# Optimization experiments

Measured on AMD Instinct MI355X. Metric: run time of the kernel, lower is better.

The kernel has to match this reference:

```python
import jax, jax.numpy as jnp
import numpy as np

N = 50000          # nodes
E = 1600000        # edges (avg degree 32)
D_MODEL = 128      # input == output dim
HEADS = 4
D_HEAD = D_MODEL // HEADS
N_LAYERS = 3


def _edge_softmax(scores, dst, n):
    # scores: [E, H]; softmax over edges sharing the same destination node
    m = jax.ops.segment_max(scores, dst, num_segments=n)          # [N, H]
    m = jnp.where(jnp.isfinite(m), m, 0.0)                        # empty segments -> -inf guard
    ex = jnp.exp(scores - m[dst])                                 # [E, H]
    denom = jax.ops.segment_sum(ex, dst, num_segments=n)          # [N, H]
    return ex / (denom[dst] + 1e-9)


def _gt_layer(h, src, dst, Wq, Wk, Wv, Wo):
    # h: [N, D]; one multi-head graph-attention (graph transformer) layer
    n = h.shape[0]
    q = (h @ Wq).reshape(n, HEADS, D_HEAD)
    k = (h @ Wk).reshape(n, HEADS, D_HEAD)
    v = (h @ Wv).reshape(n, HEADS, D_HEAD)
    scale = 1.0 / np.sqrt(D_HEAD).astype(np.float32)
    scores = jnp.einsum('ehd,ehd->eh', q[dst], k[src]) * scale    # [E, H]
    alpha = _edge_softmax(scores, dst, n)                         # [E, H]
    agg = jax.ops.segment_sum(alpha[:, :, None] * v[src], dst, num_segments=n)  # [N, H, Dh]
    return agg.reshape(n, D_MODEL) @ Wo


def setup_inputs() -> dict:
    key = jax.random.key(0)
    ks = jax.random.split(key, 16)
    s = 1.0 / np.sqrt(D_MODEL)
    inp = {
        'X':    jax.random.normal(ks[0], (N, 1), jnp.float32),
        'Seed': jax.random.uniform(ks[1], (N, 1), jnp.float32),
        'D':    jax.random.uniform(ks[2], (N, 1), jnp.float32),
        'C':    jax.random.uniform(ks[3], (N, 1), jnp.float32),
        'edge_src': jax.random.randint(ks[4], (E,), 0, N, jnp.int32),
        'edge_dst': jax.random.randint(ks[5], (E,), 0, N, jnp.int32),
        # scalar -> d_model embeddings (Linear(1, d, bias=False))
        'W_seed': jax.random.normal(ks[6], (1, D_MODEL), jnp.float32),
        'W_deg':  jax.random.normal(ks[7], (1, D_MODEL), jnp.float32),
        'W_clu':  jax.random.normal(ks[8], (1, D_MODEL), jnp.float32),
        # 3 graph-transformer layers
        'Wq': jax.random.normal(ks[9],  (N_LAYERS, D_MODEL, D_MODEL), jnp.float32) * s,
        'Wk': jax.random.normal(ks[10], (N_LAYERS, D_MODEL, D_MODEL), jnp.float32) * s,
        'Wv': jax.random.normal(ks[11], (N_LAYERS, D_MODEL, D_MODEL), jnp.float32) * s,
        'Wo': jax.random.normal(ks[12], (N_LAYERS, D_MODEL, D_MODEL), jnp.float32) * s,
        # MLP head: Linear(d,d)+ReLU, Linear(d,1)
        'W1': jax.random.normal(ks[13], (D_MODEL, D_MODEL), jnp.float32) * s,
        'b1': jnp.zeros((D_MODEL,), jnp.float32),
        'W2': jax.random.normal(ks[14], (D_MODEL, 1), jnp.float32) * s,
        'b2': jnp.zeros((1,), jnp.float32),
    }
    return inp


def reference(X, Seed, D, C, edge_src, edge_dst,
              W_seed, W_deg, W_clu, Wq, Wk, Wv, Wo, W1, b1, W2, b2):
    # faithful to original: raw X [N,1] broadcast-added to the embeddings
    h = X + Seed @ W_seed + D @ W_deg + C @ W_clu                 # [N, D_MODEL]
    for i in range(N_LAYERS):
        h = _gt_layer(h, edge_src, edge_dst, Wq[i], Wk[i], Wv[i], Wo[i])
    z = jax.nn.relu(h @ W1 + b1)
    return z @ W2 + b2                                            # [N, 1]
```

## Files before the change

### kernel.cpp

```cpp
#include <hip/hip_runtime.h>
#include <math.h>

#define DM 128
#define HEADS 4
#define DH 32
#define WSTRIDE 16384

typedef _Float16 f16x8 __attribute__((ext_vector_type(8)));
typedef _Float16 f16x4 __attribute__((ext_vector_type(4)));
typedef _Float16 f16x2 __attribute__((ext_vector_type(2)));
typedef float f32x4v __attribute__((ext_vector_type(4)));

__global__ void embed_kernel(const float* __restrict__ X, const float* __restrict__ Seed,
                             const float* __restrict__ Dg, const float* __restrict__ Cl,
                             const float* __restrict__ Wseed, const float* __restrict__ Wdeg,
                             const float* __restrict__ Wclu, float* __restrict__ H, int n) {
    int i = blockIdx.x * blockDim.x + threadIdx.x;
    if (i >= n * (DM / 4)) return;
    int nd = i >> 5, d4 = (i & 31) * 4;
    float x = X[nd], sd = Seed[nd], dg = Dg[nd], cl = Cl[nd];
    float4 ws = *reinterpret_cast<const float4*>(Wseed + d4);
    float4 wd = *reinterpret_cast<const float4*>(Wdeg + d4);
    float4 wc = *reinterpret_cast<const float4*>(Wclu + d4);
    float4 o;
    o.x = x + sd * ws.x + dg * wd.x + cl * wc.x;
    o.y = x + sd * ws.y + dg * wd.y + cl * wc.y;
    o.z = x + sd * ws.z + dg * wd.z + cl * wc.z;
    o.w = x + sd * ws.w + dg * wd.w + cl * wc.w;
    *reinterpret_cast<float4*>(H + nd * DM + d4) = o;
}

__global__ void count_kernel(const int* __restrict__ edst, int* __restrict__ deg, int E) {
    int e = blockIdx.x * blockDim.x + threadIdx.x;
    if (e < E) atomicAdd(&deg[edst[e]], 1);
}

__global__ void scan1_kernel(const int* __restrict__ in, int* __restrict__ outv,
                             int* __restrict__ bsums, int n) {
    __shared__ int s[256];
    int t = threadIdx.x;
    int i = blockIdx.x * 256 + t;
    int v = (i < n) ? in[i] : 0;
    s[t] = v;
    __syncthreads();
    for (int off = 1; off < 256; off <<= 1) {
        int x = (t >= off) ? s[t - off] : 0;
        __syncthreads();
        s[t] += x;
        __syncthreads();
    }
    if (i < n) outv[i] = s[t];
    if (t == 255) bsums[blockIdx.x] = s[255];
}

__global__ void scan2_kernel(int* __restrict__ bsums, int nb) {
    __shared__ int s[256];
    int t = threadIdx.x;
    int v = (t < nb) ? bsums[t] : 0;
    s[t] = v;
    __syncthreads();
    for (int off = 1; off < 256; off <<= 1) {
        int x = (t >= off) ? s[t - off] : 0;
        __syncthreads();
        s[t] += x;
        __syncthreads();
    }
    if (t < nb) bsums[t] = s[t];
}

__global__ void scan3_kernel(const int* __restrict__ outv, const int* __restrict__ bsums,
                             int* __restrict__ ptr, int n) {
    int i = blockIdx.x * 256 + threadIdx.x;
    if (i == 0) ptr[0] = 0;
    if (i < n) {
        int add = (blockIdx.x > 0) ? bsums[blockIdx.x - 1] : 0;
        ptr[i + 1] = outv[i] + add;
    }
}

__global__ void scatter_kernel(const int* __restrict__ esrc, const int* __restrict__ edst,
                               const int* __restrict__ ptr, int* __restrict__ fill,
                               int* __restrict__ out, int E) {
    int e = blockIdx.x * blockDim.x + threadIdx.x;
    if (e >= E) return;
    int d = edst[e];
    int pos = ptr[d] + atomicAdd(&fill[d], 1);
    out[pos] = esrc[e];
}

__global__ void prepack_kernel(const float* __restrict__ Wq, const float* __restrict__ Wk,
                               const float* __restrict__ Wv, const float* __restrict__ Wo,
                               const float* __restrict__ W1, _Float16* __restrict__ W16) {
    int m = blockIdx.z;
    const float* W;
    if (m < 3)       W = Wq + (size_t)m * DM * DM;
    else if (m < 6)  W = Wk + (size_t)(m - 3) * DM * DM;
    else if (m < 9)  W = Wv + (size_t)(m - 6) * DM * DM;
    else if (m < 12) W = Wo + (size_t)(m - 9) * DM * DM;
    else             W = W1;
    int kb = blockIdx.x, nb = blockIdx.y, l = threadIdx.x;
    int kbase = kb * 32 + (l >> 4) * 8;
    int c = nb * 16 + (l & 15);
    f16x8 v;
#pragma unroll
    for (int j = 0; j < 8; j++) v[j] = (_Float16)W[(kbase + j) * DM + c];
    *reinterpret_cast<f16x8*>(W16 + (size_t)m * WSTRIDE + ((kb * 8 + nb) * 64 + l) * 8) = v;
}

template <int OUT>
__global__ __launch_bounds__(256) void gemm_mfma_kernel(const float* __restrict__ A,
                                                        const _Float16* __restrict__ W16,
                                                        void* __restrict__ O, int ldO,
                                                        int colOff, int n) {
    __shared__ _Float16 sA[64 * 136];
    int t = threadIdx.x;
    int row0 = blockIdx.x * 64;
#pragma unroll
    for (int p = 0; p < 8; p++) {
        int f = p * 256 + t;
        int r = f >> 5, c4 = (f & 31) * 4;
        int gr = min(row0 + r, n - 1);
        float4 v = *reinterpret_cast<const float4*>(A + (size_t)gr * DM + c4);
        f16x4 h = {(_Float16)v.x, (_Float16)v.y, (_Float16)v.z, (_Float16)v.w};
        *reinterpret_cast<f16x4*>(&sA[r * 136 + c4]) = h;
    }
    __syncthreads();

    int w = t >> 6, l = t & 63;
    int lr = l & 15, lg = l >> 4;
    int rowb = w * 16;

    f32x4v acc[8];
#pragma unroll
    for (int nb = 0; nb < 8; nb++) acc[nb] = (f32x4v){0.f, 0.f, 0.f, 0.f};

#pragma unroll
    for (int kb = 0; kb < 4; kb++) {
        f16x8 a = *reinterpret_cast<const f16x8*>(&sA[(rowb + lr) * 136 + kb * 32 + lg * 8]);
#pragma unroll
        for (int nb = 0; nb < 8; nb++) {
            f16x8 b = *reinterpret_cast<const f16x8*>(&W16[((kb * 8 + nb) * 64 + l) * 8]);
            acc[nb] = __builtin_amdgcn_mfma_f32_16x16x32_f16(a, b, acc[nb], 0, 0, 0);
        }
    }

#pragma unroll
    for (int nb = 0; nb < 8; nb++) {
#pragma unroll
        for (int i = 0; i < 4; i++) {
            int r = row0 + rowb + lg * 4 + i;
            if (r >= n) continue;
            int c = nb * 16 + lr;
            if (OUT == 0) {
                ((float*)O)[(size_t)r * ldO + c] = acc[nb][i];
            } else {
                _Float16 h = (_Float16)acc[nb][i];
                ((unsigned short*)O)[(size_t)r * ldO + colOff + c] =
                    __builtin_bit_cast(unsigned short, h);
            }
        }
    }
}

__global__ __launch_bounds__(256) void attn_kernel(const float* __restrict__ Q,
                                                   const uint32_t* __restrict__ KV,
                                                   const int* __restrict__ ptr,
                                                   const int* __restrict__ esrc,
                                                   float* __restrict__ AGG, int n) {
    int w = threadIdx.x >> 6;
    int lane = threadIdx.x & 63;
    int node = blockIdx.x * 4 + w;
    if (node >= n) return;
    int e0 = ptr[node], e1 = ptr[node + 1];
    float2* outp = reinterpret_cast<float2*>(AGG + (size_t)node * DM + 2 * lane);
    if (e0 >= e1) {
        *outp = make_float2(0.f, 0.f);
        return;
    }
    const float scale = 0.17677669529663687f * 1.4426950408889634f;
    float2 qf = *reinterpret_cast<const float2*>(Q + (size_t)node * DM + 2 * lane);
    f16x2 qh = {(_Float16)qf.x, (_Float16)qf.y};

    float mA = -INFINITY, sA = 0.f, axA = 0.f, ayA = 0.f;
    float mB = -INFINITY, sB = 0.f, axB = 0.f, ayB = 0.f;

    int cnt = e1 - e0;
    int npairs = cnt >> 1;
    int last = e1 - 1;

    auto kvrow = [&](int src) { return KV + (size_t)src * 128; };

    int iA2 = 0, iB2 = 0;
    uint32_t kA0 = 0, vA0 = 0, kB0 = 0, vB0 = 0;
    uint32_t kA1 = 0, vA1 = 0, kB1 = 0, vB1 = 0;
    {
        int b0 = e0;
        int iA0 = esrc[min(b0, last)];
        int iB0 = esrc[min(b0 + 1, last)];
        const uint32_t* rA = kvrow(iA0);
        const uint32_t* rB = kvrow(iB0);
        kA0 = rA[lane]; vA0 = rA[64 + lane];
        kB0 = rB[lane]; vB0 = rB[64 + lane];
        int b1 = e0 + 2;
        int iA1 = esrc[min(b1, last)];
        int iB1 = esrc[min(b1 + 1, last)];
        const uint32_t* rA1 = kvrow(iA1);
        const uint32_t* rB1 = kvrow(iB1);
        kA1 = rA1[lane]; vA1 = rA1[64 + lane];
        kB1 = rB1[lane]; vB1 = rB1[64 + lane];
        int b2 = e0 + 4;
        iA2 = esrc[min(b2, last)];
        iB2 = esrc[min(b2 + 1, last)];
    }

#define PROC(kc, vc, m_, s_, ax_, ay_)                                         \
    {                                                                          \
        float p = __builtin_amdgcn_fdot2(qh, __builtin_bit_cast(f16x2, kc),    \
                                         0.f, false);                          \
        p += __shfl_xor(p, 1, 64);                                             \
        p += __shfl_xor(p, 2, 64);                                             \
        p += __shfl_xor(p, 4, 64);                                             \
        p += __shfl_xor(p, 8, 64);                                             \
        p *= scale;                                                            \
        float mn = fmaxf(m_, p);                                               \
        float dd = exp2f(m_ - mn);                                             \
        float wg = exp2f(p - mn);                                              \
        f16x2 vh = __builtin_bit_cast(f16x2, vc);                              \
        s_ = s_ * dd + wg;                                                     \
        ax_ = ax_ * dd + wg * (float)vh[0];                                    \
        ay_ = ay_ * dd + wg * (float)vh[1];                                    \
        m_ = mn;                                                               \
    }

    for (int p = 0; p < npairs; p++) {
        uint32_t kAc = kA0, vAc = vA0, kBc = kB0, vBc = vB0;
        kA0 = kA1; vA0 = vA1; kB0 = kB1; vB0 = vB1;
        const uint32_t* rA = kvrow(iA2);
        const uint32_t* rB = kvrow(iB2);
        kA1 = rA[lane]; vA1 = rA[64 + lane];
        kB1 = rB[lane]; vB1 = rB[64 + lane];
        int b = e0 + 2 * (p + 3);
        iA2 = esrc[min(b, last)];
        iB2 = esrc[min(b + 1, last)];
        PROC(kAc, vAc, mA, sA, axA, ayA);
        PROC(kBc, vBc, mB, sB, axB, ayB);
    }
    if (cnt & 1) {
        const uint32_t* r = kvrow(esrc[last]);
        uint32_t kc = r[lane], vc = r[64 + lane];
        PROC(kc, vc, mA, sA, axA, ayA);
    }
#undef PROC

    float mF = fmaxf(mA, mB);
    float dA = (mA > -INFINITY) ? exp2f(mA - mF) : 0.f;
    float dB = (mB > -INFINITY) ? exp2f(mB - mF) : 0.f;
    float s = sA * dA + sB * dB;
    float ax = axA * dA + axB * dB;
    float ay = ayA * dA + ayB * dB;
    float inv = 1.f / (s + 1e-9f);
    *outp = make_float2(ax * inv, ay * inv);
}

__global__ __launch_bounds__(256) void mlp_kernel(const float* __restrict__ H,
                                                  const _Float16* __restrict__ W16,
                                                  const float* __restrict__ b1,
                                                  const float* __restrict__ W2,
                                                  const float* __restrict__ b2,
                                                  float* __restrict__ out, int n) {
    __shared__ _Float16 sA[64 * 136];
    int t = threadIdx.x;
    int row0 = blockIdx.x * 64;
#pragma unroll
    for (int p = 0; p < 8; p++) {
        int f = p * 256 + t;
        int r = f >> 5, c4 = (f & 31) * 4;
        int gr = min(row0 + r, n - 1);
        float4 v = *reinterpret_cast<const float4*>(H + (size_t)gr * DM + c4);
        f16x4 h = {(_Float16)v.x, (_Float16)v.y, (_Float16)v.z, (_Float16)v.w};
        *reinterpret_cast<f16x4*>(&sA[r * 136 + c4]) = h;
    }
    __syncthreads();

    int w = t >> 6, l = t & 63;
    int lr = l & 15, lg = l >> 4;
    int rowb = w * 16;

    f32x4v acc[8];
#pragma unroll
    for (int nb = 0; nb < 8; nb++) acc[nb] = (f32x4v){0.f, 0.f, 0.f, 0.f};

#pragma unroll
    for (int kb = 0; kb < 4; kb++) {
        f16x8 a = *reinterpret_cast<const f16x8*>(&sA[(rowb + lr) * 136 + kb * 32 + lg * 8]);
#pragma unroll
        for (int nb = 0; nb < 8; nb++) {
            f16x8 b = *reinterpret_cast<const f16x8*>(&W16[((kb * 8 + nb) * 64 + l) * 8]);
            acc[nb] = __builtin_amdgcn_mfma_f32_16x16x32_f16(a, b, acc[nb], 0, 0, 0);
        }
    }

    float part[4] = {0.f, 0.f, 0.f, 0.f};
#pragma unroll
    for (int nb = 0; nb < 8; nb++) {
        int c = nb * 16 + lr;
        float b1v = b1[c];
        float w2v = W2[c];
#pragma unroll
        for (int i = 0; i < 4; i++) {
            float z = fmaxf(acc[nb][i] + b1v, 0.f);
            part[i] += z * w2v;
        }
    }
    float b2v = b2[0];
#pragma unroll
    for (int i = 0; i < 4; i++) {
        part[i] += __shfl_xor(part[i], 1, 64);
        part[i] += __shfl_xor(part[i], 2, 64);
        part[i] += __shfl_xor(part[i], 4, 64);
        part[i] += __shfl_xor(part[i], 8, 64);
        int r = row0 + rowb + lg * 4 + i;
        if (lr == 0 && r < n) out[r] = part[i] + b2v;
    }
}

extern "C" void kernel_launch(void* const* d_in, const int* in_sizes, int n_in,
                              void* d_out, int out_size, void* d_ws, size_t ws_size,
                              hipStream_t stream) {
    const float* X    = (const float*)d_in[0];
    const float* Seed = (const float*)d_in[1];
    const float* Dg   = (const float*)d_in[2];
    const float* Cl   = (const float*)d_in[3];
    const int* esrc   = (const int*)d_in[4];
    const int* edst   = (const int*)d_in[5];
    const float* Wseed = (const float*)d_in[6];
    const float* Wdeg  = (const float*)d_in[7];
    const float* Wclu  = (const float*)d_in[8];
    const float* Wq = (const float*)d_in[9];
    const float* Wk = (const float*)d_in[10];
    const float* Wv = (const float*)d_in[11];
    const float* Wo = (const float*)d_in[12];
    const float* W1 = (const float*)d_in[13];
    const float* b1 = (const float*)d_in[14];
    const float* W2 = (const float*)d_in[15];
    const float* b2 = (const float*)d_in[16];
    float* out = (float*)d_out;

    int n = in_sizes[0];
    int E = in_sizes[4];

    char* p = (char*)d_ws;
    auto alloc = [&](size_t bytes) {
        void* r = (void*)p;
        p += (bytes + 255) & ~(size_t)255;
        return r;
    };
    float* hbuf  = (float*)alloc((size_t)n * DM * 4);
    float* qbuf  = (float*)alloc((size_t)n * DM * 4);
    float* abuf  = (float*)alloc((size_t)n * DM * 4);
    unsigned short* kvbuf = (unsigned short*)alloc((size_t)n * 256 * 2);
    _Float16* W16 = (_Float16*)alloc((size_t)13 * WSTRIDE * 2);
    int* deg    = (int*)alloc((size_t)n * 4);
    int* ptr    = (int*)alloc((size_t)(n + 1) * 4);
    int* ptrtmp = (int*)alloc((size_t)n * 4);
    int* bsums  = (int*)alloc(1024);
    int* fill   = (int*)alloc((size_t)n * 4);
    int* esrcs  = (int*)alloc((size_t)E * 4);
    (void)ws_size; (void)n_in; (void)out_size;

    hipMemsetAsync(deg, 0, (size_t)n * 4, stream);
    hipMemsetAsync(fill, 0, (size_t)n * 4, stream);

    {
        int total = n * (DM / 4);
        embed_kernel<<<(total + 255) / 256, 256, 0, stream>>>(X, Seed, Dg, Cl, Wseed, Wdeg,
                                                              Wclu, hbuf, n);
    }
    int nb = (n + 255) / 256;
    count_kernel<<<(E + 255) / 256, 256, 0, stream>>>(edst, deg, E);
    scan1_kernel<<<nb, 256, 0, stream>>>(deg, ptrtmp, bsums, n);
    scan2_kernel<<<1, 256, 0, stream>>>(bsums, nb);
    scan3_kernel<<<nb, 256, 0, stream>>>(ptrtmp, bsums, ptr, n);
    scatter_kernel<<<(E + 255) / 256, 256, 0, stream>>>(esrc, edst, ptr, fill, esrcs, E);

    prepack_kernel<<<dim3(4, 8, 13), 64, 0, stream>>>(Wq, Wk, Wv, Wo, W1, W16);

    int ggrid = (n + 63) / 64;
    int agrid = (n + 3) / 4;
    for (int i = 0; i < 3; i++) {
        const _Float16* wq16 = W16 + (size_t)(0 + i) * WSTRIDE;
        const _Float16* wk16 = W16 + (size_t)(3 + i) * WSTRIDE;
        const _Float16* wv16 = W16 + (size_t)(6 + i) * WSTRIDE;
        const _Float16* wo16 = W16 + (size_t)(9 + i) * WSTRIDE;
        gemm_mfma_kernel<0><<<ggrid, 256, 0, stream>>>(hbuf, wq16, qbuf, DM, 0, n);
        gemm_mfma_kernel<1><<<ggrid, 256, 0, stream>>>(hbuf, wk16, kvbuf, 256, 0, n);
        gemm_mfma_kernel<1><<<ggrid, 256, 0, stream>>>(hbuf, wv16, kvbuf, 256, 128, n);
        attn_kernel<<<agrid, 256, 0, stream>>>(qbuf, (const uint32_t*)kvbuf, ptr, esrcs,
                                               abuf, n);
        gemm_mfma_kernel<0><<<ggrid, 256, 0, stream>>>(abuf, wo16, hbuf, DM, 0, n);
    }
    mlp_kernel<<<ggrid, 256, 0, stream>>>(hbuf, W16 + (size_t)12 * WSTRIDE, b1, W2, b2, out, n);
}
```

Measured before the change: 815.0 us.

## Process four edges per wavefront with 16-byte KV loads and lazy max rescaling

Restructures the attention kernel so each wavefront handles four edges at once, one per 16-lane quarter, with each lane holding 8 head dims loaded as uint4. The head dot-product reduction uses DPP xor adds over 4 lanes instead of four cross-lane shuffles, and the online-softmax running max is rescaled only when some new score exceeds it by more than a threshold. Partial softmax states are merged across quarters at the end. The aim is fewer shuffles, fewer exp calls and wider memory transactions per edge, at the cost of more registers and lane-divergent tail handling.

```diff
diff --git a/kernel.cpp b/kernel.cpp
--- a/kernel.cpp
+++ b/kernel.cpp
@@ -10,6 +10,15 @@
 typedef _Float16 f16x4 __attribute__((ext_vector_type(4)));
 typedef _Float16 f16x2 __attribute__((ext_vector_type(2)));
 typedef float f32x4v __attribute__((ext_vector_type(4)));
+
+__device__ __forceinline__ float dpp_xor1_add(float x) {
+    int r = __builtin_amdgcn_update_dpp(0, __builtin_bit_cast(int, x), 0xB1, 0xf, 0xf, true);
+    return x + __builtin_bit_cast(float, r);
+}
+__device__ __forceinline__ float dpp_xor2_add(float x) {
+    int r = __builtin_amdgcn_update_dpp(0, __builtin_bit_cast(int, x), 0x4E, 0xf, 0xf, true);
+    return x + __builtin_bit_cast(float, r);
+}
 
 __global__ void embed_kernel(const float* __restrict__ X, const float* __restrict__ Seed,
                              const float* __restrict__ Dg, const float* __restrict__ Cl,
@@ -167,99 +176,130 @@
                                                    const int* __restrict__ ptr,
                                                    const int* __restrict__ esrc,
                                                    float* __restrict__ AGG, int n) {
-    int w = threadIdx.x >> 6;
+    int wv = threadIdx.x >> 6;
     int lane = threadIdx.x & 63;
-    int node = blockIdx.x * 4 + w;
+    int node = blockIdx.x * 4 + wv;
     if (node >= n) return;
     int e0 = ptr[node], e1 = ptr[node + 1];
-    float2* outp = reinterpret_cast<float2*>(AGG + (size_t)node * DM + 2 * lane);
+    int q4 = lane >> 4;
+    int w = lane & 15;
+    float* outbase = AGG + (size_t)node * DM + 8 * w;
     if (e0 >= e1) {
-        *outp = make_float2(0.f, 0.f);
+        if (lane < 16) {
+            *reinterpret_cast<float4*>(outbase) = make_float4(0.f, 0.f, 0.f, 0.f);
+            *reinterpret_cast<float4*>(outbase + 4) = make_float4(0.f, 0.f, 0.f, 0.f);
+        }
         return;
     }
     const float scale = 0.17677669529663687f * 1.4426950408889634f;
-    float2 qf = *reinterpret_cast<const float2*>(Q + (size_t)node * DM + 2 * lane);
-    f16x2 qh = {(_Float16)qf.x, (_Float16)qf.y};
-
-    float mA = -INFINITY, sA = 0.f, axA = 0.f, ayA = 0.f;
-    float mB = -INFINITY, sB = 0.f, axB = 0.f, ayB = 0.f;
-
-    int cnt = e1 - e0;
-    int npairs = cnt >> 1;
+    float4 qa = *reinterpret_cast<const float4*>(Q + (size_t)node * DM + 8 * w);
+    float4 qb = *reinterpret_cast<const float4*>(Q + (size_t)node * DM + 8 * w + 4);
+    f16x2 qh0 = {(_Float16)(qa.x * scale), (_Float16)(qa.y * scale)};
+    f16x2 qh1 = {(_Float16)(qa.z * scale), (_Float16)(qa.w * scale)};
+    f16x2 qh2 = {(_Float16)(qb.x * scale), (_Float16)(qb.y * scale)};
+    f16x2 qh3 = {(_Float16)(qb.z * scale), (_Float16)(qb.w * scale)};
+
+    float m = -1e30f, s = 0.f;
+    float a0 = 0.f, a1 = 0.f, a2 = 0.f, a3 = 0.f, a4 = 0.f, a5 = 0.f, a6 = 0.f, a7 = 0.f;
+
     int last = e1 - 1;
-
-    auto kvrow = [&](int src) { return KV + (size_t)src * 128; };
-
-    int iA2 = 0, iB2 = 0;
-    uint32_t kA0 = 0, vA0 = 0, kB0 = 0, vB0 = 0;
-    uint32_t kA1 = 0, vA1 = 0, kB1 = 0, vB1 = 0;
+    int niter = (e1 - e0 + 3) >> 2;
+    int niter2 = (niter + 1) >> 1;
+
+    const uint32_t* kvw = KV + w * 4;
+
+    uint4 k0, v0, k1, v1;
     {
-        int b0 = e0;
-        int iA0 = esrc[min(b0, last)];
-        int iB0 = esrc[min(b0 + 1, last)];
-        const uint32_t* rA = kvrow(iA0);
-        const uint32_t* rB = kvrow(iB0);
-        kA0 = rA[lane]; vA0 = rA[64 + lane];
-        kB0 = rB[lane]; vB0 = rB[64 + lane];
-        int b1 = e0 + 2;
-        int iA1 = esrc[min(b1, last)];
-        int iB1 = esrc[min(b1 + 1, last)];
-        const uint32_t* rA1 = kvrow(iA1);
-        const uint32_t* rB1 = kvrow(iB1);
-        kA1 = rA1[lane]; vA1 = rA1[64 + lane];
-        kB1 = rB1[lane]; vB1 = rB1[64 + lane];
-        int b2 = e0 + 4;
-        iA2 = esrc[min(b2, last)];
-        iB2 = esrc[min(b2 + 1, last)];
-    }
-
-#define PROC(kc, vc, m_, s_, ax_, ay_)                                         \
-    {                                                                          \
-        float p = __builtin_amdgcn_fdot2(qh, __builtin_bit_cast(f16x2, kc),    \
-                                         0.f, false);                          \
-        p += __shfl_xor(p, 1, 64);                                             \
-        p += __shfl_xor(p, 2, 64);                                             \
-        p += __shfl_xor(p, 4, 64);                                             \
-        p += __shfl_xor(p, 8, 64);                                             \
-        p *= scale;                                                            \
-        float mn = fmaxf(m_, p);                                               \
-        float dd = exp2f(m_ - mn);                                             \
-        float wg = exp2f(p - mn);                                              \
-        f16x2 vh = __builtin_bit_cast(f16x2, vc);                              \
-        s_ = s_ * dd + wg;                                                     \
-        ax_ = ax_ * dd + wg * (float)vh[0];                                    \
-        ay_ = ay_ * dd + wg * (float)vh[1];                                    \
-        m_ = mn;                                                               \
-    }
-
-    for (int p = 0; p < npairs; p++) {
-        uint32_t kAc = kA0, vAc = vA0, kBc = kB0, vBc = vB0;
-        kA0 = kA1; vA0 = vA1; kB0 = kB1; vB0 = vB1;
-        const uint32_t* rA = kvrow(iA2);
-        const uint32_t* rB = kvrow(iB2);
-        kA1 = rA[lane]; vA1 = rA[64 + lane];
-        kB1 = rB[lane]; vB1 = rB[64 + lane];
-        int b = e0 + 2 * (p + 3);
-        iA2 = esrc[min(b, last)];
-        iB2 = esrc[min(b + 1, last)];
-        PROC(kAc, vAc, mA, sA, axA, ayA);
-        PROC(kBc, vBc, mB, sB, axB, ayB);
-    }
-    if (cnt & 1) {
-        const uint32_t* r = kvrow(esrc[last]);
-        uint32_t kc = r[lane], vc = r[64 + lane];
-        PROC(kc, vc, mA, sA, axA, ayA);
-    }
-#undef PROC
-
-    float mF = fmaxf(mA, mB);
-    float dA = (mA > -INFINITY) ? exp2f(mA - mF) : 0.f;
-    float dB = (mB > -INFINITY) ? exp2f(mB - mF) : 0.f;
-    float s = sA * dA + sB * dB;
-    float ax = axA * dA + axB * dB;
-    float ay = ayA * dA + ayB * dB;
+        int i0 = esrc[min(e0 + q4, last)];
+        const uint32_t* r0 = kvw + (size_t)i0 * 128;
+        k0 = *reinterpret_cast<const uint4*>(r0);
+        v0 = *reinterpret_cast<const uint4*>(r0 + 64);
+        int i1 = esrc[min(e0 + 4 + q4, last)];
+        const uint32_t* r1 = kvw + (size_t)i1 * 128;
+        k1 = *reinterpret_cast<const uint4*>(r1);
+        v1 = *reinterpret_cast<const uint4*>(r1 + 64);
+    }
+    int idx2 = esrc[min(e0 + 8 + q4, last)];
+
+#define APROC(kc, vc, bidx)                                                            \
+    {                                                                                  \
+        float p = __builtin_amdgcn_fdot2(qh0, __builtin_bit_cast(f16x2, (kc).x), 0.f, false); \
+        p = __builtin_amdgcn_fdot2(qh1, __builtin_bit_cast(f16x2, (kc).y), p, false);  \
+        p = __builtin_amdgcn_fdot2(qh2, __builtin_bit_cast(f16x2, (kc).z), p, false);  \
+        p = __builtin_amdgcn_fdot2(qh3, __builtin_bit_cast(f16x2, (kc).w), p, false);  \
+        p = dpp_xor1_add(p);                                                           \
+        p = dpp_xor2_add(p);                                                           \
+        p = ((bidx) < e1) ? p : -3.0e38f;                                              \
+        float diff = p - m;                                                            \
+        if (__any(diff > 8.f)) {                                                       \
+            float mn = fmaxf(m, p);                                                    \
+            float dd = exp2f(m - mn);                                                  \
+            s *= dd;                                                                   \
+            a0 *= dd; a1 *= dd; a2 *= dd; a3 *= dd;                                    \
+            a4 *= dd; a5 *= dd; a6 *= dd; a7 *= dd;                                    \
+            m = mn;                                                                    \
+            diff = p - m;                                                              \
+        }                                                                              \
+        float wg = exp2f(diff);                                                        \
+        s += wg;                                                                       \
+        f16x2 vh0 = __builtin_bit_cast(f16x2, (vc).x);                                 \
+        f16x2 vh1 = __builtin_bit_cast(f16x2, (vc).y);                                 \
+        f16x2 vh2 = __builtin_bit_cast(f16x2, (vc).z);                                 \
+        f16x2 vh3 = __builtin_bit_cast(f16x2, (vc).w);                                 \
+        a0 += wg * (float)vh0[0]; a1 += wg * (float)vh0[1];                            \
+        a2 += wg * (float)vh1[0]; a3 += wg * (float)vh1[1];                            \
+        a4 += wg * (float)vh2[0]; a5 += wg * (float)vh2[1];                            \
+        a6 += wg * (float)vh3[0]; a7 += wg * (float)vh3[1];                            \
+    }
+
+    int b = e0 + q4;
+    for (int it = 0; it < niter2; it++) {
+        {
+            uint4 kc = k0, vc = v0;
+            const uint32_t* r = kvw + (size_t)idx2 * 128;
+            k0 = *reinterpret_cast<const uint4*>(r);
+            v0 = *reinterpret_cast<const uint4*>(r + 64);
+            idx2 = esrc[min(b + 12, last)];
+            APROC(kc, vc, b);
+            b += 4;
+        }
+        {
+            uint4 kc = k1, vc = v1;
+            const uint32_t* r = kvw + (size_t)idx2 * 128;
+            k1 = *reinterpret_cast<const uint4*>(r);
+            v1 = *reinterpret_cast<const uint4*>(r + 64);
+            idx2 = esrc[min(b + 12, last)];
+            APROC(kc, vc, b);
+            b += 4;
+        }
+    }
+#undef APROC
+
+#pragma unroll
+    for (int off = 16; off <= 32; off <<= 1) {
+        float m2 = __shfl_xor(m, off, 64);
+        float s2 = __shfl_xor(s, off, 64);
+        float b0 = __shfl_xor(a0, off, 64), b1 = __shfl_xor(a1, off, 64);
+        float b2 = __shfl_xor(a2, off, 64), b3 = __shfl_xor(a3, off, 64);
+        float b4 = __shfl_xor(a4, off, 64), b5 = __shfl_xor(a5, off, 64);
+        float b6 = __shfl_xor(a6, off, 64), b7 = __shfl_xor(a7, off, 64);
+        float mF = fmaxf(m, m2);
+        float d1 = exp2f(m - mF), d2 = exp2f(m2 - mF);
+        s = s * d1 + s2 * d2;
+        a0 = a0 * d1 + b0 * d2; a1 = a1 * d1 + b1 * d2;
+        a2 = a2 * d1 + b2 * d2; a3 = a3 * d1 + b3 * d2;
+        a4 = a4 * d1 + b4 * d2; a5 = a5 * d1 + b5 * d2;
+        a6 = a6 * d1 + b6 * d2; a7 = a7 * d1 + b7 * d2;
+        m = mF;
+    }
+
     float inv = 1.f / (s + 1e-9f);
-    *outp = make_float2(ax * inv, ay * inv);
+    if (lane < 16) {
+        *reinterpret_cast<float4*>(outbase) =
+            make_float4(a0 * inv, a1 * inv, a2 * inv, a3 * inv);
+        *reinterpret_cast<float4*>(outbase + 4) =
+            make_float4(a4 * inv, a5 * inv, a6 * inv, a7 * inv);
+    }
 }
 
 __global__ __launch_bounds__(256) void mlp_kernel(const float* __restrict__ H,
```

Result: faster. 716.9 us (-12.0%).
